# Kernel optimization log

Measured on AMD Instinct MI355X. Metric: run time of the kernel, lower is better.

## Reference

```python
import jax, jax.numpy as jnp
import numpy as np

D_MODEL = 1024
NUM_HEADS = 16
DILATION_RATES = [2, 2, 2]
SEGMENT_SIZES = [64, 128, 256]
BATCH = 2
SEQ_LEN = 8192
N_LAYERS = len(SEGMENT_SIZES)


def setup_inputs() -> dict:
    key = jax.random.key(0)
    ks = jax.random.split(key, 5)
    d = D_MODEL
    scale = 1.0 / np.sqrt(d)
    x = jax.random.normal(ks[0], (BATCH, SEQ_LEN, d), dtype=jnp.float32)
    # Per-layer fused QKV + output projection params (stacked over layers)
    Wqkv = jax.random.normal(ks[1], (N_LAYERS, d, 3 * d), dtype=jnp.float32) * scale
    bqkv = jnp.zeros((N_LAYERS, 3 * d), dtype=jnp.float32)
    Wo = jax.random.normal(ks[2], (N_LAYERS, d, d), dtype=jnp.float32) * scale
    bo = jnp.zeros((N_LAYERS, d), dtype=jnp.float32)
    return {"x": x, "Wqkv": Wqkv, "bqkv": bqkv, "Wo": Wo, "bo": bo}


def _dilated_attention(x, Wqkv, bqkv, Wo, bo, seg, dr):
    # x: [B, S, D]. Segment, then dilate-stride within each segment.
    B, S, D = x.shape
    H = NUM_HEADS
    hd = D // H
    x4 = x.reshape(B, S // seg, seg, D)[:, :, ::dr, :]  # [B, N, s, D], s = seg//dr
    s = seg // dr
    N = S // seg
    qkv = jnp.einsum('bnsd,de->bnse', x4, Wqkv) + bqkv  # [B, N, s, 3D]
    q, k, v = jnp.split(qkv, 3, axis=-1)
    q = q.reshape(B, N, s, H, hd)
    k = k.reshape(B, N, s, H, hd)
    v = v.reshape(B, N, s, H, hd)
    # attention within each dilated segment
    scores = jnp.einsum('bnqhd,bnkhd->bnhqk', q, k) * (1.0 / np.sqrt(hd))
    attn = jax.nn.softmax(scores, axis=-1)
    o = jnp.einsum('bnhqk,bnkhd->bnqhd', attn, v).reshape(B, N, s, D)
    o = jnp.einsum('bnsd,de->bnse', o, Wo) + bo
    return o.reshape(B, N * s, D)  # [B, S/dr, D]


def reference(x, Wqkv, bqkv, Wo, bo):
    outs = []
    for i in range(N_LAYERS):
        outs.append(_dilated_attention(x, Wqkv[i], bqkv[i], Wo[i], bo[i],
                                       SEGMENT_SIZES[i], DILATION_RATES[i]))
    return jnp.stack(outs, axis=0).sum(axis=0)
```

## Files before the change

### kernel.cpp

```cpp
#include <hip/hip_runtime.h>
#include <hip/hip_bf16.h>
#include <stdint.h>

typedef unsigned short u16;
typedef short bf16x8 __attribute__((ext_vector_type(8)));
typedef u16   u16x8  __attribute__((ext_vector_type(8)));
typedef u16   u16x4  __attribute__((ext_vector_type(4)));
typedef float f32x4  __attribute__((ext_vector_type(4)));

__device__ inline u16 f2bf(float f) {
    uint32_t u = __builtin_bit_cast(uint32_t, f);
    uint32_t r = (u + 0x7FFFu + ((u >> 16) & 1u)) >> 16;
    return (u16)r;
}

__device__ inline void gload16(const void* g, void* l) {
    __builtin_amdgcn_global_load_lds((const __attribute__((address_space(1))) void*)g,
                                     (__attribute__((address_space(3))) void*)l, 16, 0, 0);
}

__device__ inline void pin_barrier() {
    __builtin_amdgcn_sched_barrier(0);
    __builtin_amdgcn_s_barrier();
    __builtin_amdgcn_sched_barrier(0);
}

#define MFMA16(a, b, c) __builtin_amdgcn_mfma_f32_16x16x32_bf16((a), (b), (c), 0, 0, 0)

__global__ __launch_bounds__(256) void k_prep_xe(const float* __restrict__ x,
                                                 u16* __restrict__ xe) {
    int row = blockIdx.x;
    int b = row >> 12, tt = row & 4095;
    const float* src = x + ((size_t)b * 8192 + 2 * (size_t)tt) * 1024;
    float4 v = ((const float4*)src)[threadIdx.x];
    u16x4 o = { f2bf(v.x), f2bf(v.y), f2bf(v.z), f2bf(v.w) };
    *(u16x4*)(xe + (size_t)row * 1024 + threadIdx.x * 4) = o;
}

__global__ __launch_bounds__(256) void k_transpose_cast(
    const float* __restrict__ src, u16* __restrict__ dst,
    int srcCols, size_t srcLayerStride, int dstStride, int dstRowPer, int dstColPer) {
    int k0 = blockIdx.x * 64, e0 = blockIdx.y * 64, layer = blockIdx.z;
    const float* s = src + (size_t)layer * srcLayerStride;
    __shared__ u16 T[64][66];
    int t = threadIdx.x;
#pragma unroll
    for (int p = 0; p < 16; ++p) {
        int l = p * 256 + t;
        int kl = l >> 6, el = l & 63;
        T[kl][el] = f2bf(s[(size_t)(k0 + kl) * srcCols + e0 + el]);
    }
    __syncthreads();
    int rowBase = layer * dstRowPer + e0;
    int colBase = layer * dstColPer + k0;
#pragma unroll
    for (int p = 0; p < 16; ++p) {
        int l = p * 256 + t;
        int eo = l >> 6, ko = l & 63;
        dst[(size_t)(rowBase + eo) * dstStride + colBase + ko] = T[ko][eo];
    }
}

template <int BN, bool BF16OUT>
__global__ __launch_bounds__(512, 2) void k_gemm4(
    const u16* __restrict__ A, const u16* __restrict__ B, void* __restrict__ C,
    const float* __restrict__ bias0, const float* __restrict__ bias1,
    const float* __restrict__ bias2, int K, int lda, int ldb, int ldc,
    int gxmask, int gxshift) {
    constexpr int WN = BN / 64;
    constexpr int WM = 8 / WN;
    constexpr int MFRAG = 256 / (WM * 16);
    constexpr int NB = BN / 64;
    constexpr int BUFSZ = 32768 + BN * 128;

    __shared__ __align__(16) char smem[131072];
    const int tid = threadIdx.x, lane = tid & 63, wave = tid >> 6;
    const int wr = wave / WN, wc = wave % WN;

    const int nwg = gridDim.x, bid = blockIdx.x;
    const int cpx = nwg >> 3;
    const int swz = (bid & 7) * cpx + (bid >> 3);
    const int bx = swz & gxmask, by = swz >> gxshift;
    const int row0 = bx << 8, col0 = by * BN;

    const size_t lda2 = (size_t)lda * 2, ldb2 = (size_t)ldb * 2;
    const char* pA0 = (const char*)A +
        (size_t)(row0 + wave * 8 + (lane >> 3)) * lda2 + ((lane & 7) ^ (lane >> 3)) * 16;
    const char* pB0 = (const char*)B +
        (size_t)(col0 + wave * 8 + (lane >> 3)) * ldb2 + ((lane & 7) ^ (lane >> 3)) * 16;

#define STA(i, sb, kof) gload16(pA0 + (size_t)(i) * 64 * lda2 + (kof), (sb) + ((i) * 8 + wave) * 1024)
#define STB(i, sb, kof) gload16(pB0 + (size_t)(i) * 64 * ldb2 + (kof), (sb) + 32768 + ((i) * 8 + wave) * 1024)

    const int la = lane & 15, lg = lane >> 4, l7 = lane & 7;
    const int offK0 = la * 128 + ((lg ^ l7) << 4);
    const int offK1 = la * 128 + (((4 + lg) ^ l7) << 4);

    f32x4 acc[MFRAG][4] = {};
    const int nt = K >> 6;

    char* const BUF0 = smem;
    char* const BUF1 = smem + BUFSZ;

    {
#pragma unroll
        for (int i = 0; i < 4; ++i) STA(i, BUF0, 0);
#pragma unroll
        for (int i = 0; i < NB; ++i) STB(i, BUF0, 0);
        __builtin_amdgcn_sched_barrier(0);
        asm volatile("s_waitcnt vmcnt(0)" ::: "memory");
        pin_barrier();
    }

    for (int t = 0; t < nt; ++t) {
        char* rq = (t & 1) ? BUF1 : BUF0;
        char* sq = (t & 1) ? BUF0 : BUF1;
        const bool st = (t + 1 < nt);
        const size_t kof = (size_t)(t + 1) * 128;
        const char* aB = rq + wr * (MFRAG * 2048);
        const char* bB = rq + 32768 + wc * 8192;

        bf16x8 af[4], ag[4], b0[4], b1[4];
#pragma unroll
        for (int n = 0; n < 4; ++n) b0[n] = *(const bf16x8*)(bB + n * 2048 + offK0);
#pragma unroll
        for (int m = 0; m < 4; ++m) af[m] = *(const bf16x8*)(aB + m * 2048 + offK0);
        if (st) { STA(0, sq, kof); STA(1, sq, kof); }
#pragma unroll
        for (int m = 0; m < 4; ++m)
            ag[m] = *(const bf16x8*)(aB + 8192 + m * 2048 + offK0);
#pragma unroll
        for (int n = 0; n < 4; ++n) b1[n] = *(const bf16x8*)(bB + n * 2048 + offK1);
        if (st) {
            STA(2, sq, kof); STA(3, sq, kof);
#pragma unroll
            for (int i = 0; i < NB; ++i) STB(i, sq, kof);
        }
        __builtin_amdgcn_s_setprio(1);
#pragma unroll
        for (int m = 0; m < 4; ++m)
#pragma unroll
            for (int n = 0; n < 4; ++n)
                acc[m][n] = MFMA16(af[m], b0[n], acc[m][n]);
        __builtin_amdgcn_s_setprio(0);
        __builtin_amdgcn_sched_barrier(0);
#pragma unroll
        for (int m = 0; m < 4; ++m) af[m] = *(const bf16x8*)(aB + m * 2048 + offK1);
        __builtin_amdgcn_s_setprio(1);
#pragma unroll
        for (int m = 0; m < 4; ++m)
#pragma unroll
            for (int n = 0; n < 4; ++n)
                acc[4 + m][n] = MFMA16(ag[m], b0[n], acc[4 + m][n]);
        __builtin_amdgcn_s_setprio(0);
        __builtin_amdgcn_sched_barrier(0);
#pragma unroll
        for (int m = 0; m < 4; ++m)
            ag[m] = *(const bf16x8*)(aB + 8192 + m * 2048 + offK1);
        __builtin_amdgcn_s_setprio(1);
#pragma unroll
        for (int m = 0; m < 4; ++m)
#pragma unroll
            for (int n = 0; n < 4; ++n)
                acc[m][n] = MFMA16(af[m], b1[n], acc[m][n]);
        __builtin_amdgcn_s_setprio(0);
        __builtin_amdgcn_sched_barrier(0);
        __builtin_amdgcn_s_setprio(1);
#pragma unroll
        for (int m = 0; m < 4; ++m)
#pragma unroll
            for (int n = 0; n < 4; ++n)
                acc[4 + m][n] = MFMA16(ag[m], b1[n], acc[4 + m][n]);
        __builtin_amdgcn_s_setprio(0);
        __builtin_amdgcn_sched_barrier(0);
        asm volatile("s_waitcnt vmcnt(0)" ::: "memory");
        pin_barrier();
    }
#undef STA
#undef STB

    {
        char* cst = smem;
        const int g4 = (lane >> 4) << 2, cl = lane & 15;
#pragma unroll
        for (int n = 0; n < 4; ++n) {
            int col = wc * 64 + n * 16 + cl;
            float bs = bias0[col0 + col];
            if (bias1) bs += bias1[col0 + col];
            if (bias2) bs += bias2[col0 + col];
#pragma unroll
            for (int m = 0; m < MFRAG; ++m) {
#pragma unroll
                for (int r = 0; r < 4; ++r) {
                    int row = wr * (MFRAG * 16) + m * 16 + g4 + r;
                    float v = acc[m][n][r] + bs;
                    if (BF16OUT) {
                        int scol = col ^ (((row >> 2) & 3) << 3);
                        *(u16*)(cst + row * 512 + scol * 2) = f2bf(v);
                    } else {
                        int scol = col ^ (((row >> 2) & 3) << 2);
                        *(float*)(cst + row * 512 + scol * 4) = v;
                    }
                }
            }
        }
        pin_barrier();
        const int esz = BF16OUT ? 2 : 4;
#pragma unroll
        for (int it = 0; it < 16; ++it) {
            int id = it * 512 + tid;
            int row = id >> 5, c16 = id & 31;
            int sc16 = c16 ^ ((row >> 2) & 3);
            u16x8 v = *(const u16x8*)(cst + row * 512 + sc16 * 16);
            char* dst = (char*)C + ((size_t)(row0 + row) * ldc + col0) * esz + c16 * 16;
            *(u16x8*)dst = v;
        }
    }
}

__global__ __launch_bounds__(256, 2) void k_gemm4b(
    const u16* __restrict__ A, const u16* __restrict__ B, float* __restrict__ C,
    const float* __restrict__ bias0, const float* __restrict__ bias1,
    const float* __restrict__ bias2, int K, int lda, int ldb, int ldc,
    int gxmask, int gxshift) {
    __shared__ __align__(16) char smem[65536];
    const int tid = threadIdx.x, lane = tid & 63, wave = tid >> 6;
    const int wr = wave >> 1, wc = wave & 1;

    const int nwg = gridDim.x, bid = blockIdx.x;
    const int cpx = nwg >> 3;
    const int swz = (bid & 7) * cpx + (bid >> 3);
    const int bx = swz & gxmask, by = swz >> gxshift;
    const int row0 = bx << 7, col0 = by << 7;

    const size_t lda2 = (size_t)lda * 2, ldb2 = (size_t)ldb * 2;
    const int sRow = tid >> 3;
    const int sChunk = (tid & 7) ^ (sRow & 7);
    const char* pA0 = (const char*)A + (size_t)(row0 + sRow) * lda2 + sChunk * 16;
    const char* pB0 = (const char*)B + (size_t)(col0 + sRow) * ldb2 + sChunk * 16;

#define STA_(i, sb, kof) gload16(pA0 + (size_t)(i) * 32 * lda2 + (kof), \
                                 (sb) + (i) * 4096 + wave * 1024)
#define STB_(i, sb, kof) gload16(pB0 + (size_t)(i) * 32 * ldb2 + (kof), \
                                 (sb) + 16384 + (i) * 4096 + wave * 1024)

    const int la = lane & 15, lg = lane >> 4;
    const int loff0 = la * 128 + (((lg) ^ (la & 7)) << 4);
    const int loff1 = la * 128 + (((4 + lg) ^ (la & 7)) << 4);

    f32x4 acc[4][4] = {};
    const int nt = K >> 6;

#pragma unroll
    for (int i = 0; i < 4; ++i) STA_(i, smem, 0);
#pragma unroll
    for (int i = 0; i < 4; ++i) STB_(i, smem, 0);
    __builtin_amdgcn_sched_barrier(0);
    asm volatile("s_waitcnt vmcnt(0)" ::: "memory");
    pin_barrier();

    for (int t = 0; t < nt; ++t) {
        char* rq = smem + (t & 1) * 32768;
        char* sq = smem + ((t & 1) ^ 1) * 32768;
        const bool st = (t + 1 < nt);
        const size_t kof = (size_t)(t + 1) * 128;
        const char* aB = rq + wr * 8192;
        const char* bB = rq + 16384 + wc * 8192;

        bf16x8 a0[4], a1[4], b0f[4], b1f[4];
#pragma unroll
        for (int n = 0; n < 4; ++n) b0f[n] = *(const bf16x8*)(bB + n * 2048 + loff0);
#pragma unroll
        for (int m = 0; m < 4; ++m) a0[m] = *(const bf16x8*)(aB + m * 2048 + loff0);
        if (st) { STA_(0, sq, kof); STA_(1, sq, kof); STA_(2, sq, kof); STA_(3, sq, kof); }
#pragma unroll
        for (int n = 0; n < 4; ++n) b1f[n] = *(const bf16x8*)(bB + n * 2048 + loff1);
#pragma unroll
        for (int m = 0; m < 4; ++m) a1[m] = *(const bf16x8*)(aB + m * 2048 + loff1);
        if (st) { STB_(0, sq, kof); STB_(1, sq, kof); STB_(2, sq, kof); STB_(3, sq, kof); }

        __builtin_amdgcn_sched_barrier(0);
        __builtin_amdgcn_s_setprio(1);
#pragma unroll
        for (int m = 0; m < 4; ++m)
#pragma unroll
            for (int n = 0; n < 4; ++n)
                acc[m][n] = MFMA16(a0[m], b0f[n], acc[m][n]);
        __builtin_amdgcn_s_setprio(0);
        __builtin_amdgcn_sched_barrier(0);
        __builtin_amdgcn_s_setprio(1);
#pragma unroll
        for (int m = 0; m < 4; ++m)
#pragma unroll
            for (int n = 0; n < 4; ++n)
                acc[m][n] = MFMA16(a1[m], b1f[n], acc[m][n]);
        __builtin_amdgcn_s_setprio(0);
        __builtin_amdgcn_sched_barrier(0);
        asm volatile("s_waitcnt vmcnt(0)" ::: "memory");
        pin_barrier();
    }
#undef STA_
#undef STB_

    {
        float* cst = (float*)smem;
        const int g4 = lg << 2;
#pragma unroll
        for (int n = 0; n < 4; ++n) {
            int col = wc * 64 + n * 16 + la;
            float bs = bias0[col0 + col] + bias1[col0 + col] + bias2[col0 + col];
#pragma unroll
            for (int m = 0; m < 4; ++m) {
#pragma unroll
                for (int r = 0; r < 4; ++r) {
                    int row = wr * 64 + m * 16 + g4 + r;
                    int scol = col ^ (((row >> 2) & 3) << 3);
                    cst[row * 128 + scol] = acc[m][n][r] + bs;
                }
            }
        }
        pin_barrier();
#pragma unroll
        for (int it = 0; it < 16; ++it) {
            int id = it * 256 + tid;
            int row = id >> 5, c16 = id & 31;
            int sc16 = c16 ^ (((row >> 2) & 3) << 1);
            u16x8 v = *(const u16x8*)((char*)cst + row * 512 + sc16 * 16);
            *(u16x8*)((char*)C + ((size_t)(row0 + row) * ldc + col0) * 4 + c16 * 16) = v;
        }
    }
}

template <int S>
__global__ __launch_bounds__(256) void k_attn(const u16* __restrict__ qkv,
                                              u16* __restrict__ ab, int layer) {
    constexpr int NCT = S / 16;
    constexpr int RPW = (S == 32) ? 1 : S / 64;
    constexpr int ACTIVE = (S == 32) ? 2 : 4;
    constexpr int KST = S / 32;
    constexpr int VSTRIDE = 2 * S;
    constexpr int VMASK = VSTRIDE / 16 - 1;

    __shared__ __align__(16) char KS[S * 128];
    __shared__ __align__(16) char VTS[64 * VSTRIDE];
    __shared__ __align__(16) char PS[S * VSTRIDE];

    const int per_b = (4096 / S) * 16;
    const int b = blockIdx.x / per_b;
    const int r0 = blockIdx.x % per_b;
    const int n = r0 >> 4, h = r0 & 15;
    const int token0 = b * 4096 + n * S;
    const int colQ = layer * 3072 + h * 64;
    const int tid = threadIdx.x, lane = tid & 63, wave = tid >> 6;

    constexpr int CHUNKS = S / 32;
#pragma unroll
    for (int c = 0; c < CHUNKS; ++c) {
        int lc = c * 256 + tid;
        int row = lc >> 3, off = (lc & 7) * 16;
        const char* base = (const char*)qkv + ((size_t)(token0 + row) * 9216 + colQ) * 2 + off;
        u16x8 kv = *(const u16x8*)(base + 1024 * 2);
        *(u16x8*)(KS + row * 128 + (off ^ ((row & 7) << 4))) = kv;
        u16x8 vv = *(const u16x8*)(base + 2048 * 2);
        int cb = off >> 1;
#pragma unroll
        for (int e = 0; e < 8; ++e) {
            int col = cb + e;
            *(u16*)(VTS + col * VSTRIDE + ((row * 2) ^ ((col & VMASK) << 4))) = vv[e];
        }
    }
    __syncthreads();

    f32x4 sacc[RPW][NCT] = {};
    if (wave < ACTIVE) {
#pragma unroll
        for (int rl = 0; rl < RPW; ++rl) {
            int rt = wave * RPW + rl;
#pragma unroll
            for (int ks2 = 0; ks2 < 2; ++ks2) {
                int qrow = token0 + rt * 16 + (lane & 15);
                int kbyte = ks2 * 64 + ((lane >> 4) << 4);
                bf16x8 aq = *(const bf16x8*)((const char*)qkv +
                              ((size_t)qrow * 9216 + colQ) * 2 + kbyte);
#pragma unroll
                for (int ct = 0; ct < NCT; ++ct) {
                    int krow = ct * 16 + (lane & 15);
                    bf16x8 bk = *(const bf16x8*)(KS + krow * 128 + (kbyte ^ ((krow & 7) << 4)));
                    sacc[rl][ct] = MFMA16(aq, bk, sacc[rl][ct]);
                }
            }
        }
#pragma unroll
        for (int rl = 0; rl < RPW; ++rl) {
            int rt = wave * RPW + rl;
#pragma unroll
            for (int r = 0; r < 4; ++r) {
                float vals[NCT];
                float m = -1e30f;
#pragma unroll
                for (int ct = 0; ct < NCT; ++ct) {
                    vals[ct] = sacc[rl][ct][r] * 0.125f;
                    m = fmaxf(m, vals[ct]);
                }
#pragma unroll
                for (int d = 1; d < 16; d <<= 1) m = fmaxf(m, __shfl_xor(m, d, 64));
                float sum = 0.f;
#pragma unroll
                for (int ct = 0; ct < NCT; ++ct) {
                    float p = exp2f((vals[ct] - m) * 1.44269504f);
                    vals[ct] = p;
                    sum += p;
                }
#pragma unroll
                for (int d = 1; d < 16; d <<= 1) sum += __shfl_xor(sum, d, 64);
                float inv = 1.0f / sum;
                int row = rt * 16 + ((lane >> 4) << 2) + r;
#pragma unroll
                for (int ct = 0; ct < NCT; ++ct) {
                    int col = ct * 16 + (lane & 15);
                    *(u16*)(PS + row * VSTRIDE + ((col * 2) ^ ((row & VMASK) << 4))) =
                        f2bf(vals[ct] * inv);
                }
            }
        }
    }
    __syncthreads();

    if (wave < ACTIVE) {
        const int colA = layer * 1024 + h * 64;
#pragma unroll
        for (int rl = 0; rl < RPW; ++rl) {
            int rt = wave * RPW + rl;
            f32x4 oacc[4] = {};
#pragma unroll
            for (int ks2 = 0; ks2 < KST; ++ks2) {
                int kbyte = ks2 * 64 + ((lane >> 4) << 4);
                int prow = rt * 16 + (lane & 15);
                bf16x8 ap = *(const bf16x8*)(PS + prow * VSTRIDE + (kbyte ^ ((prow & VMASK) << 4)));
#pragma unroll
                for (int ct = 0; ct < 4; ++ct) {
                    int vcol = ct * 16 + (lane & 15);
                    bf16x8 bv = *(const bf16x8*)(VTS + vcol * VSTRIDE + (kbyte ^ ((vcol & VMASK) << 4)));
                    oacc[ct] = MFMA16(ap, bv, oacc[ct]);
                }
            }
#pragma unroll
            for (int ct = 0; ct < 4; ++ct) {
#pragma unroll
                for (int r = 0; r < 4; ++r) {
                    int row = token0 + rt * 16 + ((lane >> 4) << 2) + r;
                    int col = colA + ct * 16 + (lane & 15);
                    ab[(size_t)row * 3072 + col] = f2bf(oacc[ct][r]);
                }
            }
        }
    }
}

extern "C" void kernel_launch(void* const* d_in, const int* in_sizes, int n_in,
                              void* d_out, int out_size, void* d_ws, size_t ws_size,
                              hipStream_t stream) {
    const float* x    = (const float*)d_in[0];
    const float* Wqkv = (const float*)d_in[1];
    const float* bqkv = (const float*)d_in[2];
    const float* Wo   = (const float*)d_in[3];
    const float* bo   = (const float*)d_in[4];

    char* ws = (char*)d_ws;
    u16* XE    = (u16*)(ws);
    u16* WQKVT = (u16*)(ws + 16777216);
    u16* WOT   = (u16*)(ws + 35651584);
    u16* QKVB  = (u16*)(ws + 41943040);
    u16* ABUF  = (u16*)(ws + 192937984);

    k_prep_xe<<<8192, 256, 0, stream>>>(x, XE);
    k_transpose_cast<<<dim3(16, 48, 3), 256, 0, stream>>>(
        Wqkv, WQKVT, 3072, (size_t)1024 * 3072, 1024, 3072, 0);
    k_transpose_cast<<<dim3(16, 16, 3), 256, 0, stream>>>(
        Wo, WOT, 1024, (size_t)1024 * 1024, 3072, 0, 1024);

    k_gemm4<256, true><<<dim3(1152), 512, 0, stream>>>(
        XE, WQKVT, QKVB, bqkv, nullptr, nullptr, 1024, 1024, 1024, 9216, 31, 5);

    k_attn<32><<<4096, 256, 0, stream>>>(QKVB, ABUF, 0);
    k_attn<64><<<2048, 256, 0, stream>>>(QKVB, ABUF, 1);
    k_attn<128><<<1024, 256, 0, stream>>>(QKVB, ABUF, 2);

    k_gemm4b<<<dim3(512), 256, 0, stream>>>(
        ABUF, WOT, (float*)d_out, bo, bo + 1024, bo + 2048,
        3072, 3072, 3072, 1024, 63, 6);
}
```

Baseline: 317.3 us.

## Halve output GEMM LDS footprint for higher occupancy; pack two heads per attention block

The output-projection GEMM now uses a K-step of 32 instead of 64, halving LDS from 64KB to 32KB so four workgroups can fit per CU. The epilogue stages the 128x128 tile in two 64-row halves to fit the smaller buffer. The S=32 attention kernel now processes two heads per block so all four waves are busy instead of two, halving its grid. The trade-off is more loop iterations and barriers per K in the GEMM, for better latency hiding through occupancy.

```diff
diff --git a/kernel.cpp b/kernel.cpp
--- a/kernel.cpp
+++ b/kernel.cpp
@@ -218,12 +218,12 @@
     }
 }
 
-__global__ __launch_bounds__(256, 2) void k_gemm4b(
+__global__ __launch_bounds__(256, 4) void k_gemm4c(
     const u16* __restrict__ A, const u16* __restrict__ B, float* __restrict__ C,
     const float* __restrict__ bias0, const float* __restrict__ bias1,
     const float* __restrict__ bias2, int K, int lda, int ldb, int ldc,
     int gxmask, int gxshift) {
-    __shared__ __align__(16) char smem[65536];
+    __shared__ __align__(16) char smem[32768];
     const int tid = threadIdx.x, lane = tid & 63, wave = tid >> 6;
     const int wr = wave >> 1, wc = wave & 1;
 
@@ -234,50 +234,41 @@
     const int row0 = bx << 7, col0 = by << 7;
 
     const size_t lda2 = (size_t)lda * 2, ldb2 = (size_t)ldb * 2;
-    const int sRow = tid >> 3;
-    const int sChunk = (tid & 7) ^ (sRow & 7);
-    const char* pA0 = (const char*)A + (size_t)(row0 + sRow) * lda2 + sChunk * 16;
-    const char* pB0 = (const char*)B + (size_t)(col0 + sRow) * ldb2 + sChunk * 16;
-
-#define STA_(i, sb, kof) gload16(pA0 + (size_t)(i) * 32 * lda2 + (kof), \
-                                 (sb) + (i) * 4096 + wave * 1024)
-#define STB_(i, sb, kof) gload16(pB0 + (size_t)(i) * 32 * ldb2 + (kof), \
-                                 (sb) + 16384 + (i) * 4096 + wave * 1024)
+    const int cSw = ((tid & 3) ^ ((tid >> 3) & 3)) * 16;
+    const char* pA0 = (const char*)A + (size_t)(row0 + (tid >> 2)) * lda2 + cSw;
+    const char* pB0 = (const char*)B + (size_t)(col0 + (tid >> 2)) * ldb2 + cSw;
+
+#define STA_(i, sb, kof) gload16(pA0 + (size_t)(i) * 64 * lda2 + (kof), \
+                                 (sb) + (i) * 4096 + tid * 16)
+#define STB_(i, sb, kof) gload16(pB0 + (size_t)(i) * 64 * ldb2 + (kof), \
+                                 (sb) + 8192 + (i) * 4096 + tid * 16)
 
     const int la = lane & 15, lg = lane >> 4;
-    const int loff0 = la * 128 + (((lg) ^ (la & 7)) << 4);
-    const int loff1 = la * 128 + (((4 + lg) ^ (la & 7)) << 4);
+    const int loff = la * 64 + ((lg ^ ((la >> 1) & 3)) << 4);
 
     f32x4 acc[4][4] = {};
-    const int nt = K >> 6;
-
-#pragma unroll
-    for (int i = 0; i < 4; ++i) STA_(i, smem, 0);
-#pragma unroll
-    for (int i = 0; i < 4; ++i) STB_(i, smem, 0);
+    const int nt = K >> 5;
+
+    STA_(0, smem, 0); STA_(1, smem, 0);
+    STB_(0, smem, 0); STB_(1, smem, 0);
     __builtin_amdgcn_sched_barrier(0);
     asm volatile("s_waitcnt vmcnt(0)" ::: "memory");
     pin_barrier();
 
     for (int t = 0; t < nt; ++t) {
-        char* rq = smem + (t & 1) * 32768;
-        char* sq = smem + ((t & 1) ^ 1) * 32768;
+        char* rq = smem + (t & 1) * 16384;
+        char* sq = smem + ((t & 1) ^ 1) * 16384;
         const bool st = (t + 1 < nt);
-        const size_t kof = (size_t)(t + 1) * 128;
-        const char* aB = rq + wr * 8192;
-        const char* bB = rq + 16384 + wc * 8192;
-
-        bf16x8 a0[4], a1[4], b0f[4], b1f[4];
-#pragma unroll
-        for (int n = 0; n < 4; ++n) b0f[n] = *(const bf16x8*)(bB + n * 2048 + loff0);
-#pragma unroll
-        for (int m = 0; m < 4; ++m) a0[m] = *(const bf16x8*)(aB + m * 2048 + loff0);
-        if (st) { STA_(0, sq, kof); STA_(1, sq, kof); STA_(2, sq, kof); STA_(3, sq, kof); }
-#pragma unroll
-        for (int n = 0; n < 4; ++n) b1f[n] = *(const bf16x8*)(bB + n * 2048 + loff1);
-#pragma unroll
-        for (int m = 0; m < 4; ++m) a1[m] = *(const bf16x8*)(aB + m * 2048 + loff1);
-        if (st) { STB_(0, sq, kof); STB_(1, sq, kof); STB_(2, sq, kof); STB_(3, sq, kof); }
+        const size_t kof = (size_t)(t + 1) * 64;
+        const char* aB = rq + wr * 4096;
+        const char* bB = rq + 8192 + wc * 4096;
+
+        bf16x8 af[4], bf[4];
+#pragma unroll
+        for (int n = 0; n < 4; ++n) bf[n] = *(const bf16x8*)(bB + n * 1024 + loff);
+#pragma unroll
+        for (int m = 0; m < 4; ++m) af[m] = *(const bf16x8*)(aB + m * 1024 + loff);
+        if (st) { STA_(0, sq, kof); STA_(1, sq, kof); STB_(0, sq, kof); STB_(1, sq, kof); }
 
         __builtin_amdgcn_sched_barrier(0);
         __builtin_amdgcn_s_setprio(1);
@@ -285,15 +276,7 @@
         for (int m = 0; m < 4; ++m)
 #pragma unroll
             for (int n = 0; n < 4; ++n)
-                acc[m][n] = MFMA16(a0[m], b0f[n], acc[m][n]);
-        __builtin_amdgcn_s_setprio(0);
-        __builtin_amdgcn_sched_barrier(0);
-        __builtin_amdgcn_s_setprio(1);
-#pragma unroll
-        for (int m = 0; m < 4; ++m)
-#pragma unroll
-            for (int n = 0; n < 4; ++n)
-                acc[m][n] = MFMA16(a1[m], b1f[n], acc[m][n]);
+                acc[m][n] = MFMA16(af[m], bf[n], acc[m][n]);
         __builtin_amdgcn_s_setprio(0);
         __builtin_amdgcn_sched_barrier(0);
         asm volatile("s_waitcnt vmcnt(0)" ::: "memory");
@@ -306,32 +289,39 @@
         float* cst = (float*)smem;
         const int g4 = lg << 2;
 #pragma unroll
-        for (int n = 0; n < 4; ++n) {
-            int col = wc * 64 + n * 16 + la;
-            float bs = bias0[col0 + col] + bias1[col0 + col] + bias2[col0 + col];
-#pragma unroll
-            for (int m = 0; m < 4; ++m) {
-#pragma unroll
-                for (int r = 0; r < 4; ++r) {
-                    int row = wr * 64 + m * 16 + g4 + r;
-                    int scol = col ^ (((row >> 2) & 3) << 3);
-                    cst[row * 128 + scol] = acc[m][n][r] + bs;
-                }
-            }
-        }
-        pin_barrier();
-#pragma unroll
-        for (int it = 0; it < 16; ++it) {
-            int id = it * 256 + tid;
-            int row = id >> 5, c16 = id & 31;
-            int sc16 = c16 ^ (((row >> 2) & 3) << 1);
-            u16x8 v = *(const u16x8*)((char*)cst + row * 512 + sc16 * 16);
-            *(u16x8*)((char*)C + ((size_t)(row0 + row) * ldc + col0) * 4 + c16 * 16) = v;
-        }
-    }
-}
-
-template <int S>
+        for (int p = 0; p < 2; ++p) {
+            if (wr == p) {
+#pragma unroll
+                for (int n = 0; n < 4; ++n) {
+                    int col = wc * 64 + n * 16 + la;
+                    float bs = bias0[col0 + col] + bias1[col0 + col] + bias2[col0 + col];
+#pragma unroll
+                    for (int m = 0; m < 4; ++m) {
+#pragma unroll
+                        for (int r = 0; r < 4; ++r) {
+                            int row = m * 16 + g4 + r;
+                            int scol = col ^ (((row >> 2) & 3) << 3);
+                            cst[row * 128 + scol] = acc[m][n][r] + bs;
+                        }
+                    }
+                }
+            }
+            pin_barrier();
+#pragma unroll
+            for (int it = 0; it < 8; ++it) {
+                int id = it * 256 + tid;
+                int row = id >> 5, c16 = id & 31;
+                int sc16 = c16 ^ (((row >> 2) & 3) << 1);
+                u16x8 v = *(const u16x8*)((char*)cst + row * 512 + sc16 * 16);
+                *(u16x8*)((char*)C + ((size_t)(row0 + p * 64 + row) * ldc + col0) * 4
+                          + c16 * 16) = v;
+            }
+            pin_barrier();
+        }
+    }
+}
+
+template <int S, int HP>
 __global__ __launch_bounds__(256) void k_attn(const u16* __restrict__ qkv,
                                               u16* __restrict__ ab, int layer) {
     constexpr int NCT = S / 16;
@@ -340,42 +330,49 @@
     constexpr int KST = S / 32;
     constexpr int VSTRIDE = 2 * S;
     constexpr int VMASK = VSTRIDE / 16 - 1;
-
-    __shared__ __align__(16) char KS[S * 128];
-    __shared__ __align__(16) char VTS[64 * VSTRIDE];
-    __shared__ __align__(16) char PS[S * VSTRIDE];
-
-    const int per_b = (4096 / S) * 16;
+    constexpr int HPB = 16 / HP;
+
+    __shared__ __align__(16) char KS[HP][S * 128];
+    __shared__ __align__(16) char VTS[HP][64 * VSTRIDE];
+    __shared__ __align__(16) char PS[HP][S * VSTRIDE];
+
+    const int per_b = (4096 / S) * HPB;
     const int b = blockIdx.x / per_b;
     const int r0 = blockIdx.x % per_b;
-    const int n = r0 >> 4, h = r0 & 15;
+    const int n = r0 / HPB, hbase = (r0 % HPB) * HP;
     const int token0 = b * 4096 + n * S;
-    const int colQ = layer * 3072 + h * 64;
     const int tid = threadIdx.x, lane = tid & 63, wave = tid >> 6;
+    const int hp = (HP == 2) ? (wave >> 1) : 0;
+    const int lw = (HP == 2) ? (wave & 1) : wave;
 
     constexpr int CHUNKS = S / 32;
 #pragma unroll
-    for (int c = 0; c < CHUNKS; ++c) {
-        int lc = c * 256 + tid;
-        int row = lc >> 3, off = (lc & 7) * 16;
-        const char* base = (const char*)qkv + ((size_t)(token0 + row) * 9216 + colQ) * 2 + off;
-        u16x8 kv = *(const u16x8*)(base + 1024 * 2);
-        *(u16x8*)(KS + row * 128 + (off ^ ((row & 7) << 4))) = kv;
-        u16x8 vv = *(const u16x8*)(base + 2048 * 2);
-        int cb = off >> 1;
-#pragma unroll
-        for (int e = 0; e < 8; ++e) {
-            int col = cb + e;
-            *(u16*)(VTS + col * VSTRIDE + ((row * 2) ^ ((col & VMASK) << 4))) = vv[e];
+    for (int hs = 0; hs < HP; ++hs) {
+        const int colQ = layer * 3072 + (hbase + hs) * 64;
+#pragma unroll
+        for (int c = 0; c < CHUNKS; ++c) {
+            int lc = c * 256 + tid;
+            int row = lc >> 3, off = (lc & 7) * 16;
+            const char* base = (const char*)qkv + ((size_t)(token0 + row) * 9216 + colQ) * 2 + off;
+            u16x8 kv = *(const u16x8*)(base + 1024 * 2);
+            *(u16x8*)(KS[hs] + row * 128 + (off ^ ((row & 7) << 4))) = kv;
+            u16x8 vv = *(const u16x8*)(base + 2048 * 2);
+            int cb = off >> 1;
+#pragma unroll
+            for (int e = 0; e < 8; ++e) {
+                int col = cb + e;
+                *(u16*)(VTS[hs] + col * VSTRIDE + ((row * 2) ^ ((col & VMASK) << 4))) = vv[e];
+            }
         }
     }
     __syncthreads();
 
+    const int colQ = layer * 3072 + (hbase + hp) * 64;
     f32x4 sacc[RPW][NCT] = {};
-    if (wave < ACTIVE) {
+    if (lw < ACTIVE) {
 #pragma unroll
         for (int rl = 0; rl < RPW; ++rl) {
-            int rt = wave * RPW + rl;
+            int rt = lw * RPW + rl;
 #pragma unroll
             for (int ks2 = 0; ks2 < 2; ++ks2) {
                 int qrow = token0 + rt * 16 + (lane & 15);
@@ -385,14 +382,14 @@
 #pragma unroll
                 for (int ct = 0; ct < NCT; ++ct) {
                     int krow = ct * 16 + (lane & 15);
-                    bf16x8 bk = *(const bf16x8*)(KS + krow * 128 + (kbyte ^ ((krow & 7) << 4)));
+                    bf16x8 bk = *(const bf16x8*)(KS[hp] + krow * 128 + (kbyte ^ ((krow & 7) << 4)));
                     sacc[rl][ct] = MFMA16(aq, bk, sacc[rl][ct]);
                 }
             }
         }
 #pragma unroll
         for (int rl = 0; rl < RPW; ++rl) {
-            int rt = wave * RPW + rl;
+            int rt = lw * RPW + rl;
 #pragma unroll
             for (int r = 0; r < 4; ++r) {
                 float vals[NCT];
@@ -418,7 +415,7 @@
 #pragma unroll
                 for (int ct = 0; ct < NCT; ++ct) {
                     int col = ct * 16 + (lane & 15);
-                    *(u16*)(PS + row * VSTRIDE + ((col * 2) ^ ((row & VMASK) << 4))) =
+                    *(u16*)(PS[hp] + row * VSTRIDE + ((col * 2) ^ ((row & VMASK) << 4))) =
                         f2bf(vals[ct] * inv);
                 }
             }
@@ -426,21 +423,21 @@
     }
     __syncthreads();
 
-    if (wave < ACTIVE) {
-        const int colA = layer * 1024 + h * 64;
+    if (lw < ACTIVE) {
+        const int colA = layer * 1024 + (hbase + hp) * 64;
 #pragma unroll
         for (int rl = 0; rl < RPW; ++rl) {
-            int rt = wave * RPW + rl;
+            int rt = lw * RPW + rl;
             f32x4 oacc[4] = {};
 #pragma unroll
             for (int ks2 = 0; ks2 < KST; ++ks2) {
                 int kbyte = ks2 * 64 + ((lane >> 4) << 4);
                 int prow = rt * 16 + (lane & 15);
-                bf16x8 ap = *(const bf16x8*)(PS + prow * VSTRIDE + (kbyte ^ ((prow & VMASK) << 4)));
+                bf16x8 ap = *(const bf16x8*)(PS[hp] + prow * VSTRIDE + (kbyte ^ ((prow & VMASK) << 4)));
 #pragma unroll
                 for (int ct = 0; ct < 4; ++ct) {
                     int vcol = ct * 16 + (lane & 15);
-                    bf16x8 bv = *(const bf16x8*)(VTS + vcol * VSTRIDE + (kbyte ^ ((vcol & VMASK) << 4)));
+                    bf16x8 bv = *(const bf16x8*)(VTS[hp] + vcol * VSTRIDE + (kbyte ^ ((vcol & VMASK) << 4)));
                     oacc[ct] = MFMA16(ap, bv, oacc[ct]);
                 }
             }
@@ -482,11 +479,11 @@
     k_gemm4<256, true><<<dim3(1152), 512, 0, stream>>>(
         XE, WQKVT, QKVB, bqkv, nullptr, nullptr, 1024, 1024, 1024, 9216, 31, 5);
 
-    k_attn<32><<<4096, 256, 0, stream>>>(QKVB, ABUF, 0);
-    k_attn<64><<<2048, 256, 0, stream>>>(QKVB, ABUF, 1);
-    k_attn<128><<<1024, 256, 0, stream>>>(QKVB, ABUF, 2);
-
-    k_gemm4b<<<dim3(512), 256, 0, stream>>>(
+    k_attn<32, 2><<<2048, 256, 0, stream>>>(QKVB, ABUF, 0);
+    k_attn<64, 1><<<2048, 256, 0, stream>>>(QKVB, ABUF, 1);
+    k_attn<128, 1><<<1024, 256, 0, stream>>>(QKVB, ABUF, 2);
+
+    k_gemm4c<<<dim3(512), 256, 0, stream>>>(
         ABUF, WOT, (float*)d_out, bo, bo + 1024, bo + 2048,
         3072, 3072, 3072, 1024, 63, 6);
 }
```

Measured after the change: 321.7 us. Within noise of the previous version (+1.4%).
